# Kernel optimization log

Hardware: AMD Instinct MI355X
Metric: run time of the kernel (lower is better)

Reference implementation:

```python
import jax, jax.numpy as jnp
import numpy as np

N = 12288
D = 128
NUM_BATCH = 32
EPS = 1e-8


def setup_inputs() -> dict:
    key = jax.random.key(0)
    kq, kk, kv, kb = jax.random.split(key, 4)
    Q = jax.random.normal(kq, (N, D), dtype=jnp.float32)
    K = jax.random.normal(kk, (N, D), dtype=jnp.float32)
    V = jax.random.normal(kv, (N, D), dtype=jnp.float32)
    batch_seg = jnp.sort(jax.random.randint(kb, (N,), 0, NUM_BATCH, dtype=jnp.int32))
    return {"Q": Q, "K": K, "V": V, "num_batch": NUM_BATCH, "batch_seg": batch_seg}


def reference(Q, K, V, num_batch, batch_seg):
    d = Q.shape[-1]
    dot = Q @ K.T                                   # [N, N]
    # NOTE: faithful to original: subtract GLOBAL max, then divide by sqrt(d)
    A = jnp.exp((dot - jnp.max(dot)) / jnp.sqrt(jnp.float32(d)))
    if num_batch > 1:
        mask = (batch_seg[None, :] == batch_seg[:, None])  # block-diagonal
        A = jnp.where(mask, A, jnp.zeros((), A.dtype))
    norm = jnp.sum(A, axis=-1, keepdims=True) + EPS
    A_weights = A / norm
    return A_weights @ V
```

## Files before the change

kernel.cpp:

```cpp
#include <hip/hip_runtime.h>


#define NN 12288
#define DD 128
#define NB 32
#define PS_LD 40
#define VTS 12424

typedef __attribute__((ext_vector_type(8))) short short8;
typedef __attribute__((ext_vector_type(4))) float float4v;

__device__ __forceinline__ short f2bf(float f) {
  unsigned u = __builtin_bit_cast(unsigned, f);
  return (short)((u + 0x7FFFu + ((u >> 16) & 1u)) >> 16);
}

__device__ __forceinline__ short8 ld8_bf16(const float* p) {
  float4v f0 = *(const float4v*)p;
  float4v f1 = *(const float4v*)(p + 4);
  short8 s;
  s[0] = f2bf(f0[0]); s[1] = f2bf(f0[1]); s[2] = f2bf(f0[2]); s[3] = f2bf(f0[3]);
  s[4] = f2bf(f1[0]); s[5] = f2bf(f1[1]); s[6] = f2bf(f1[2]); s[7] = f2bf(f1[3]);
  return s;
}

__global__ __launch_bounds__(256) void prep_kernel(
    const float* __restrict__ K, const float* __restrict__ V,
    const int* __restrict__ seg,
    short* __restrict__ Kb, short* __restrict__ Vtb, int* __restrict__ starts) {
  const int tid = threadIdx.x;
  const int b = blockIdx.x;
  if (b < 768) {
    const size_t base = (size_t)b * 2048 + (size_t)tid * 8;
    *(short8*)(Kb + base) = ld8_bf16(K + base);
  } else if (b < 864) {
    __shared__ __align__(16) short Ts[DD * 136];
    const int kt = (b - 768) * 128;
#pragma unroll
    for (int rep = 0; rep < 16; ++rep) {
      int v = rep * 256 + tid;
      int key = v >> 5, c4 = (v & 31) * 4;
      float4v f = *(const float4v*)(V + (size_t)(kt + key) * DD + c4);
      Ts[(c4 + 0) * 136 + key] = f2bf(f[0]);
      Ts[(c4 + 1) * 136 + key] = f2bf(f[1]);
      Ts[(c4 + 2) * 136 + key] = f2bf(f[2]);
      Ts[(c4 + 3) * 136 + key] = f2bf(f[3]);
    }
    __syncthreads();
    const int c16 = (tid & 15) * 8;
#pragma unroll
    for (int rep = 0; rep < 8; ++rep) {
      int d = rep * 16 + (tid >> 4);
      short8 s = *(const short8*)&Ts[d * 136 + c16];
      *(short8*)(Vtb + (size_t)d * VTS + kt + c16) = s;
    }
  } else {
    int i = (b - 864) * 256 + tid;
    int s = seg[i];
    int sp = (i == 0) ? -1 : seg[i - 1];
    for (int bb = sp + 1; bb <= s; ++bb) starts[bb] = i;
    if (i == NN - 1)
      for (int bb = s + 1; bb <= NB; ++bb) starts[bb] = NN;
  }
}

struct Frags {
  short8 k0[4];
  short8 k1[4];
  short8 v[8];
};

__device__ __forceinline__ void load_frags(
    const short* __restrict__ Kb, const short* __restrict__ Vtb,
    int j0, int c, int quad, Frags& f) {
  const short* ka = Kb + (size_t)(j0 + c) * DD + quad * 8;
  const short* kb = ka + 16 * DD;
#pragma unroll
  for (int kc = 0; kc < 4; ++kc) {
    f.k0[kc] = *(const short8*)(ka + kc * 32);
    f.k1[kc] = *(const short8*)(kb + kc * 32);
  }
  const short* vb = Vtb + (size_t)c * VTS + j0 + quad * 8;
#pragma unroll
  for (int n = 0; n < 8; ++n)
    f.v[n] = *(const short8*)(vb + (size_t)n * 16 * VTS);
}

__global__ __launch_bounds__(256, 2) void attn_kernel(
    const float* __restrict__ Q, const short* __restrict__ Kb,
    const short* __restrict__ Vtb, const int* __restrict__ seg,
    const int* __restrict__ starts, float* __restrict__ out) {
  __shared__ __align__(16) short Ps[4][16 * PS_LD];
  __shared__ __align__(16) float Osc[4][16 * DD];
  __shared__ float Ls[4][16];

  const int tid = threadIdx.x;
  const int wave = tid >> 6;
  const int lane = tid & 63;
  const int c = lane & 15;
  const int quad = lane >> 4;

  const int bid = blockIdx.x;
  const int rg = (bid & 7) * 96 + (bid >> 3);
  const int i0 = rg * 16;

  const int segLoRow = seg[i0], segHiRow = seg[i0 + 15];
  const int lo = starts[segLoRow] & ~31;
  const int hi = starts[segHiRow + 1];

  int st_r[4], en_r[4];
#pragma unroll
  for (int r = 0; r < 4; ++r) {
    int s = seg[i0 + quad * 4 + r];
    st_r[r] = starts[s];
    en_r[r] = starts[s + 1];
  }

  short8 qf[4];
  {
    const float* qrow = Q + (size_t)(i0 + c) * DD + quad * 8;
#pragma unroll
    for (int kc = 0; kc < 4; ++kc) qf[kc] = ld8_bf16(qrow + kc * 32);
  }

  float4v acc[8];
#pragma unroll
  for (int n = 0; n < 8; ++n) acc[n] = (float4v){0.f, 0.f, 0.f, 0.f};
  float l_part[4] = {0.f, 0.f, 0.f, 0.f};

  const float scale = 0.08838834764831845f;

  int j0 = lo + wave * 32;
  if (j0 < hi) {
    Frags cur, nxt;
    load_frags(Kb, Vtb, j0, c, quad, cur);
    while (j0 < hi) {
      const int jn = j0 + 128;
      const int jl = (jn < hi) ? jn : j0;
      load_frags(Kb, Vtb, jl, c, quad, nxt);

      float4v s0 = (float4v){0.f, 0.f, 0.f, 0.f};
      float4v s1 = (float4v){0.f, 0.f, 0.f, 0.f};
#pragma unroll
      for (int kc = 0; kc < 4; ++kc) {
        s0 = __builtin_amdgcn_mfma_f32_16x16x32_bf16(qf[kc], cur.k0[kc], s0, 0, 0, 0);
        s1 = __builtin_amdgcn_mfma_f32_16x16x32_bf16(qf[kc], cur.k1[kc], s1, 0, 0, 0);
      }
      const int ja = j0 + c, jb = ja + 16;
      short* prow = &Ps[wave][0];
#pragma unroll
      for (int r = 0; r < 4; ++r) {
        float pa = (ja >= st_r[r] && ja < en_r[r]) ? __expf(s0[r] * scale) : 0.f;
        float pb = (jb >= st_r[r] && jb < en_r[r]) ? __expf(s1[r] * scale) : 0.f;
        l_part[r] += pa + pb;
        int row = quad * 4 + r;
        prow[row * PS_LD + c]      = f2bf(pa);
        prow[row * PS_LD + 16 + c] = f2bf(pb);
      }
      short8 pf = *(const short8*)&Ps[wave][c * PS_LD + quad * 8];
#pragma unroll
      for (int n = 0; n < 8; ++n)
        acc[n] = __builtin_amdgcn_mfma_f32_16x16x32_bf16(pf, cur.v[n], acc[n], 0, 0, 0);

      cur = nxt;
      j0 = jn;
    }
  }

  float lrow[4];
#pragma unroll
  for (int r = 0; r < 4; ++r) {
    float l = l_part[r];
    l += __shfl_xor(l, 1, 64);
    l += __shfl_xor(l, 2, 64);
    l += __shfl_xor(l, 4, 64);
    l += __shfl_xor(l, 8, 64);
    lrow[r] = l;
  }

#pragma unroll
  for (int n = 0; n < 8; ++n)
#pragma unroll
    for (int r = 0; r < 4; ++r)
      Osc[wave][(quad * 4 + r) * DD + n * 16 + c] = acc[n][r];
  if (c == 0) {
#pragma unroll
    for (int r = 0; r < 4; ++r) Ls[wave][quad * 4 + r] = lrow[r];
  }
  __syncthreads();

#pragma unroll
  for (int rep = 0; rep < 2; ++rep) {
    int e4 = rep * 256 + tid;
    int row = e4 >> 5, c4 = (e4 & 31) * 4;
    float l = Ls[0][row] + Ls[1][row] + Ls[2][row] + Ls[3][row];
    float4v o = (float4v){0.f, 0.f, 0.f, 0.f};
#pragma unroll
    for (int w = 0; w < 4; ++w) {
      float4v t = *(const float4v*)&Osc[w][row * DD + c4];
      o[0] += t[0]; o[1] += t[1]; o[2] += t[2]; o[3] += t[3];
    }
    float inv = 1.f / (l + 1e-8f);
    o[0] *= inv; o[1] *= inv; o[2] *= inv; o[3] *= inv;
    *(float4v*)(out + (size_t)(i0 + row) * DD + c4) = o;
  }
}

#define KT_LD 136
#define VT_LD 40
typedef __attribute__((ext_vector_type(4))) short short4v;

__global__ __launch_bounds__(256) void attn_fallback(
    const float* __restrict__ Q, const float* __restrict__ K,
    const float* __restrict__ V, const int* __restrict__ seg,
    float* __restrict__ out) {
  __shared__ __align__(16) short Kt[32 * KT_LD];
  __shared__ __align__(16) short Vt[DD * VT_LD];
  __shared__ __align__(16) short Ps[4][16 * PS_LD];
  const int tid = threadIdx.x, wave = tid >> 6, lane = tid & 63;
  const int c = lane & 15, quad = lane >> 4;
  const int m0 = blockIdx.x * 64, i0 = m0 + wave * 16;
  const int segFirst = seg[m0], segLast = seg[m0 + 63];
  int lo = 0, hb = NN;
  while (lo < hb) { int mid = (lo + hb) >> 1; if (seg[mid] < segFirst) lo = mid + 1; else hb = mid; }
  int hi = lo, hb2 = NN;
  while (hi < hb2) { int mid = (hi + hb2) >> 1; if (seg[mid] <= segLast) hi = mid + 1; else hb2 = mid; }
  short8 qf[4];
  const float* qrow = Q + (size_t)(i0 + c) * DD + quad * 8;
#pragma unroll
  for (int kc = 0; kc < 4; ++kc) qf[kc] = ld8_bf16(qrow + kc * 32);
  int seg_r[4];
#pragma unroll
  for (int r = 0; r < 4; ++r) seg_r[r] = seg[i0 + quad * 4 + r];
  float4v acc[8];
#pragma unroll
  for (int n = 0; n < 8; ++n) acc[n] = (float4v){0.f, 0.f, 0.f, 0.f};
  float l_part[4] = {0.f, 0.f, 0.f, 0.f};
  const float scale = 0.08838834764831845f;
  for (int j0 = lo; j0 < hi; j0 += 32) {
    __syncthreads();
    {
      int row = tid >> 3, ch = tid & 7;
      int jj = j0 + row; if (jj > NN - 1) jj = NN - 1;
      const float* kp = K + (size_t)jj * DD + ch * 16;
      short* dst = &Kt[row * KT_LD + ch * 16];
#pragma unroll
      for (int q4 = 0; q4 < 4; ++q4) {
        float4v f = *(const float4v*)(kp + q4 * 4);
        short4v s;
        s[0] = f2bf(f[0]); s[1] = f2bf(f[1]); s[2] = f2bf(f[2]); s[3] = f2bf(f[3]);
        *(short4v*)(dst + q4 * 4) = s;
      }
    }
    {
      int d = tid & 127, jh = tid >> 7;
      float vv[16];
#pragma unroll
      for (int j = 0; j < 16; ++j) {
        int jj = j0 + jh * 16 + j; if (jj > NN - 1) jj = NN - 1;
        vv[j] = V[(size_t)jj * DD + d];
      }
      short8 a, b2;
#pragma unroll
      for (int j = 0; j < 8; ++j) { a[j] = f2bf(vv[j]); b2[j] = f2bf(vv[8 + j]); }
      *(short8*)&Vt[d * VT_LD + jh * 16] = a;
      *(short8*)&Vt[d * VT_LD + jh * 16 + 8] = b2;
    }
    __syncthreads();
    float4v s0 = (float4v){0.f, 0.f, 0.f, 0.f};
    float4v s1 = (float4v){0.f, 0.f, 0.f, 0.f};
    const short* krow0 = &Kt[c * KT_LD + quad * 8];
    const short* krow1 = &Kt[(16 + c) * KT_LD + quad * 8];
#pragma unroll
    for (int kc = 0; kc < 4; ++kc) {
      short8 b0 = *(const short8*)(krow0 + kc * 32);
      short8 b1 = *(const short8*)(krow1 + kc * 32);
      s0 = __builtin_amdgcn_mfma_f32_16x16x32_bf16(qf[kc], b0, s0, 0, 0, 0);
      s1 = __builtin_amdgcn_mfma_f32_16x16x32_bf16(qf[kc], b1, s1, 0, 0, 0);
    }
    int ja = j0 + c, jb = ja + 16;
    int sa = seg[ja < NN ? ja : NN - 1];
    int sb = seg[jb < NN ? jb : NN - 1];
    bool va = ja < hi, vb = jb < hi;
    short* prow = &Ps[wave][0];
#pragma unroll
    for (int r = 0; r < 4; ++r) {
      float pa = (va && sa == seg_r[r]) ? __expf(s0[r] * scale) : 0.f;
      float pb = (vb && sb == seg_r[r]) ? __expf(s1[r] * scale) : 0.f;
      l_part[r] += pa + pb;
      int row = quad * 4 + r;
      prow[row * PS_LD + c] = f2bf(pa);
      prow[row * PS_LD + 16 + c] = f2bf(pb);
    }
    short8 pf = *(const short8*)&Ps[wave][c * PS_LD + quad * 8];
#pragma unroll
    for (int n = 0; n < 8; ++n) {
      short8 vfr = *(const short8*)&Vt[(n * 16 + c) * VT_LD + quad * 8];
      acc[n] = __builtin_amdgcn_mfma_f32_16x16x32_bf16(pf, vfr, acc[n], 0, 0, 0);
    }
  }
  float linv[4];
#pragma unroll
  for (int r = 0; r < 4; ++r) {
    float l = l_part[r];
    l += __shfl_xor(l, 1, 64);
    l += __shfl_xor(l, 2, 64);
    l += __shfl_xor(l, 4, 64);
    l += __shfl_xor(l, 8, 64);
    linv[r] = 1.f / (l + 1e-8f);
  }
#pragma unroll
  for (int n = 0; n < 8; ++n)
#pragma unroll
    for (int r = 0; r < 4; ++r)
      out[(size_t)(i0 + quad * 4 + r) * DD + n * 16 + c] = acc[n][r] * linv[r];
}

extern "C" void kernel_launch(void* const* d_in, const int* in_sizes, int n_in,
                              void* d_out, int out_size, void* d_ws, size_t ws_size,
                              hipStream_t stream) {
  const float* Q = (const float*)d_in[0];
  const float* K = (const float*)d_in[1];
  const float* V = (const float*)d_in[2];
  const int* seg = (const int*)d_in[4];
  float* out = (float*)d_out;

  const size_t kb_bytes = (size_t)NN * DD * sizeof(short);
  const size_t vt_bytes = (size_t)DD * VTS * sizeof(short);
  const size_t need = kb_bytes + vt_bytes + 64 * sizeof(int);

  if (ws_size >= need) {
    short* Kb = (short*)d_ws;
    short* Vtb = (short*)((char*)d_ws + kb_bytes);
    int* starts = (int*)((char*)d_ws + kb_bytes + vt_bytes);
    prep_kernel<<<864 + NN / 256, 256, 0, stream>>>(K, V, seg, Kb, Vtb, starts);
    attn_kernel<<<NN / 16, 256, 0, stream>>>(Q, Kb, Vtb, seg, starts, out);
  } else {
    attn_fallback<<<NN / 64, 256, 0, stream>>>(Q, K, V, seg, out);
  }
}
```

Baseline: 106.8 us.

## Share K/V tiles across 64-row blocks via LDS DMA and split keys

Each block now covers 64 query rows (16 per wave) and stages 32-key K and V^T tiles into swizzled LDS with global_load_lds double buffering, so all four waves reuse each tile instead of each wave loading its own fragments from global memory. The key range is split four ways across blocks, and partial outputs and row sums go to a workspace that a new combine kernel reduces and normalises. This cuts redundant global K/V traffic and improves load balance. In exchange it adds an extra kernel launch, a block-wide barrier per tile, and a large fp32 partial-output write and read.

Result: faster. 96.40 us (-9.7%).

```diff
diff --git a/kernel.cpp b/kernel.cpp
--- a/kernel.cpp
+++ b/kernel.cpp
@@ -22,6 +22,12 @@
   s[0] = f2bf(f0[0]); s[1] = f2bf(f0[1]); s[2] = f2bf(f0[2]); s[3] = f2bf(f0[3]);
   s[4] = f2bf(f1[0]); s[5] = f2bf(f1[1]); s[6] = f2bf(f1[2]); s[7] = f2bf(f1[3]);
   return s;
+}
+
+__device__ __forceinline__ void dma16(const short* gsrc, short* ldst) {
+  auto g = (const __attribute__((address_space(1))) void*)(unsigned long long)gsrc;
+  auto l = (__attribute__((address_space(3))) void*)(unsigned)(unsigned long long)ldst;
+  __builtin_amdgcn_global_load_lds(g, l, 16, 0, 0);
 }
 
 __global__ __launch_bounds__(256) void prep_kernel(
@@ -64,35 +70,33 @@
   }
 }
 
-struct Frags {
-  short8 k0[4];
-  short8 k1[4];
-  short8 v[8];
-};
-
-__device__ __forceinline__ void load_frags(
+__device__ __forceinline__ void issue_tile(
     const short* __restrict__ Kb, const short* __restrict__ Vtb,
-    int j0, int c, int quad, Frags& f) {
-  const short* ka = Kb + (size_t)(j0 + c) * DD + quad * 8;
-  const short* kb = ka + 16 * DD;
-#pragma unroll
-  for (int kc = 0; kc < 4; ++kc) {
-    f.k0[kc] = *(const short8*)(ka + kc * 32);
-    f.k1[kc] = *(const short8*)(kb + kc * 32);
-  }
-  const short* vb = Vtb + (size_t)c * VTS + j0 + quad * 8;
-#pragma unroll
-  for (int n = 0; n < 8; ++n)
-    f.v[n] = *(const short8*)(vb + (size_t)n * 16 * VTS);
-}
-
-__global__ __launch_bounds__(256, 2) void attn_kernel(
+    short* KshP, short* VshP, int j0, int wave, int lane) {
+#pragma unroll
+  for (int i = 0; i < 2; ++i) {
+    const int R = wave * 8 + i * 4;
+    const int row = R + (lane >> 4);
+    const int dchunk = (lane & 15) ^ (row & 15);
+    dma16(Kb + (size_t)(j0 + row) * DD + dchunk * 8, KshP + R * 128);
+  }
+#pragma unroll
+  for (int i = 0; i < 2; ++i) {
+    const int D = wave * 32 + i * 16;
+    const int dr = D + (lane >> 2);
+    const int vchunk = (lane & 3) ^ ((lane >> 2) & 3);
+    dma16(Vtb + (size_t)dr * VTS + j0 + vchunk * 8, VshP + D * 32);
+  }
+}
+
+__global__ __launch_bounds__(256, 3) void attn_kernel(
     const float* __restrict__ Q, const short* __restrict__ Kb,
     const short* __restrict__ Vtb, const int* __restrict__ seg,
-    const int* __restrict__ starts, float* __restrict__ out) {
+    const int* __restrict__ starts,
+    float* __restrict__ Op, float* __restrict__ lp) {
+  __shared__ __align__(16) short Ksh[2][32 * 128];
+  __shared__ __align__(16) short Vsh[2][128 * 32];
   __shared__ __align__(16) short Ps[4][16 * PS_LD];
-  __shared__ __align__(16) float Osc[4][16 * DD];
-  __shared__ float Ls[4][16];
 
   const int tid = threadIdx.x;
   const int wave = tid >> 6;
@@ -101,24 +105,31 @@
   const int quad = lane >> 4;
 
   const int bid = blockIdx.x;
-  const int rg = (bid & 7) * 96 + (bid >> 3);
-  const int i0 = rg * 16;
-
-  const int segLoRow = seg[i0], segHiRow = seg[i0 + 15];
-  const int lo = starts[segLoRow] & ~31;
-  const int hi = starts[segHiRow + 1];
+  const int y = bid >> 3;
+  const int rg = (bid & 7) * 24 + (y >> 2);
+  const int sk = y & 3;
+  const int i0 = rg * 64;
+  const int i0w = i0 + wave * 16;
+
+  const int L = starts[seg[i0]];
+  const int H = starts[seg[i0 + 63] + 1];
+  const int Lm = L & ~31;
+  const int nck = (H - Lm + 31) >> 5;
+  const int ck0 = (nck * sk) >> 2;
+  const int ck1 = (nck * (sk + 1)) >> 2;
+  const int nt = ck1 - ck0;
 
   int st_r[4], en_r[4];
 #pragma unroll
   for (int r = 0; r < 4; ++r) {
-    int s = seg[i0 + quad * 4 + r];
+    int s = seg[i0w + quad * 4 + r];
     st_r[r] = starts[s];
     en_r[r] = starts[s + 1];
   }
 
   short8 qf[4];
   {
-    const float* qrow = Q + (size_t)(i0 + c) * DD + quad * 8;
+    const float* qrow = Q + (size_t)(i0w + c) * DD + quad * 8;
 #pragma unroll
     for (int kc = 0; kc < 4; ++kc) qf[kc] = ld8_bf16(qrow + kc * 32);
   }
@@ -130,41 +141,50 @@
 
   const float scale = 0.08838834764831845f;
 
-  int j0 = lo + wave * 32;
-  if (j0 < hi) {
-    Frags cur, nxt;
-    load_frags(Kb, Vtb, j0, c, quad, cur);
-    while (j0 < hi) {
-      const int jn = j0 + 128;
-      const int jl = (jn < hi) ? jn : j0;
-      load_frags(Kb, Vtb, jl, c, quad, nxt);
-
-      float4v s0 = (float4v){0.f, 0.f, 0.f, 0.f};
-      float4v s1 = (float4v){0.f, 0.f, 0.f, 0.f};
-#pragma unroll
-      for (int kc = 0; kc < 4; ++kc) {
-        s0 = __builtin_amdgcn_mfma_f32_16x16x32_bf16(qf[kc], cur.k0[kc], s0, 0, 0, 0);
-        s1 = __builtin_amdgcn_mfma_f32_16x16x32_bf16(qf[kc], cur.k1[kc], s1, 0, 0, 0);
-      }
-      const int ja = j0 + c, jb = ja + 16;
-      short* prow = &Ps[wave][0];
-#pragma unroll
-      for (int r = 0; r < 4; ++r) {
-        float pa = (ja >= st_r[r] && ja < en_r[r]) ? __expf(s0[r] * scale) : 0.f;
-        float pb = (jb >= st_r[r] && jb < en_r[r]) ? __expf(s1[r] * scale) : 0.f;
-        l_part[r] += pa + pb;
-        int row = quad * 4 + r;
-        prow[row * PS_LD + c]      = f2bf(pa);
-        prow[row * PS_LD + 16 + c] = f2bf(pb);
-      }
-      short8 pf = *(const short8*)&Ps[wave][c * PS_LD + quad * 8];
-#pragma unroll
-      for (int n = 0; n < 8; ++n)
-        acc[n] = __builtin_amdgcn_mfma_f32_16x16x32_bf16(pf, cur.v[n], acc[n], 0, 0, 0);
-
-      cur = nxt;
-      j0 = jn;
-    }
+  if (nt > 0)
+    issue_tile(Kb, Vtb, &Ksh[0][0], &Vsh[0][0], Lm + ck0 * 32, wave, lane);
+  __syncthreads();
+
+  for (int t = 0; t < nt; ++t) {
+    const int j0 = Lm + (ck0 + t) * 32;
+    const int p = t & 1;
+    if (t + 1 < nt)
+      issue_tile(Kb, Vtb, &Ksh[p ^ 1][0], &Vsh[p ^ 1][0], j0 + 32, wave, lane);
+
+    float4v s0 = (float4v){0.f, 0.f, 0.f, 0.f};
+    float4v s1 = (float4v){0.f, 0.f, 0.f, 0.f};
+    const short* Kp = &Ksh[p][0];
+#pragma unroll
+    for (int kc = 0; kc < 4; ++kc) {
+      const int pos = ((kc * 4 + quad) ^ c) * 8;
+      short8 b0 = *(const short8*)(Kp + c * 128 + pos);
+      short8 b1 = *(const short8*)(Kp + (16 + c) * 128 + pos);
+      s0 = __builtin_amdgcn_mfma_f32_16x16x32_bf16(qf[kc], b0, s0, 0, 0, 0);
+      s1 = __builtin_amdgcn_mfma_f32_16x16x32_bf16(qf[kc], b1, s1, 0, 0, 0);
+    }
+
+    const int ja = j0 + c, jb = ja + 16;
+    short* prow = &Ps[wave][0];
+#pragma unroll
+    for (int r = 0; r < 4; ++r) {
+      float pa = (ja >= st_r[r] && ja < en_r[r]) ? __expf(s0[r] * scale) : 0.f;
+      float pb = (jb >= st_r[r] && jb < en_r[r]) ? __expf(s1[r] * scale) : 0.f;
+      l_part[r] += pa + pb;
+      int row = quad * 4 + r;
+      prow[row * PS_LD + c]      = f2bf(pa);
+      prow[row * PS_LD + 16 + c] = f2bf(pb);
+    }
+    short8 pf = *(const short8*)&Ps[wave][c * PS_LD + quad * 8];
+
+    const short* Vp = &Vsh[p][0];
+    const int vpos = (quad ^ (c & 3)) * 8;
+#pragma unroll
+    for (int n = 0; n < 8; ++n) {
+      short8 vf = *(const short8*)(Vp + (n * 16 + c) * 32 + vpos);
+      acc[n] = __builtin_amdgcn_mfma_f32_16x16x32_bf16(pf, vf, acc[n], 0, 0, 0);
+    }
+
+    __syncthreads();
   }
 
   float lrow[4];
@@ -178,31 +198,36 @@
     lrow[r] = l;
   }
 
+  float* OpW = Op + ((size_t)sk * NN + i0w) * DD;
 #pragma unroll
   for (int n = 0; n < 8; ++n)
 #pragma unroll
     for (int r = 0; r < 4; ++r)
-      Osc[wave][(quad * 4 + r) * DD + n * 16 + c] = acc[n][r];
+      OpW[(quad * 4 + r) * DD + n * 16 + c] = acc[n][r];
   if (c == 0) {
 #pragma unroll
-    for (int r = 0; r < 4; ++r) Ls[wave][quad * 4 + r] = lrow[r];
-  }
-  __syncthreads();
-
+    for (int r = 0; r < 4; ++r) lp[sk * NN + i0w + quad * 4 + r] = lrow[r];
+  }
+}
+
+__global__ __launch_bounds__(256) void combine_kernel(
+    const float* __restrict__ Op, const float* __restrict__ lp,
+    float* __restrict__ out) {
+  const int idx = blockIdx.x * 256 + threadIdx.x;
 #pragma unroll
   for (int rep = 0; rep < 2; ++rep) {
-    int e4 = rep * 256 + tid;
-    int row = e4 >> 5, c4 = (e4 & 31) * 4;
-    float l = Ls[0][row] + Ls[1][row] + Ls[2][row] + Ls[3][row];
+    int u = idx + rep * 196608;
+    int row = u >> 5, c4 = (u & 31) * 4;
+    float l = lp[row] + lp[NN + row] + lp[2 * NN + row] + lp[3 * NN + row];
     float4v o = (float4v){0.f, 0.f, 0.f, 0.f};
 #pragma unroll
-    for (int w = 0; w < 4; ++w) {
-      float4v t = *(const float4v*)&Osc[w][row * DD + c4];
+    for (int s = 0; s < 4; ++s) {
+      float4v t = *(const float4v*)(Op + ((size_t)s * NN + row) * DD + c4);
       o[0] += t[0]; o[1] += t[1]; o[2] += t[2]; o[3] += t[3];
     }
     float inv = 1.f / (l + 1e-8f);
     o[0] *= inv; o[1] *= inv; o[2] *= inv; o[3] *= inv;
-    *(float4v*)(out + (size_t)(i0 + row) * DD + c4) = o;
+    *(float4v*)(out + (size_t)row * DD + c4) = o;
   }
 }
 
@@ -327,14 +352,21 @@
 
   const size_t kb_bytes = (size_t)NN * DD * sizeof(short);
   const size_t vt_bytes = (size_t)DD * VTS * sizeof(short);
-  const size_t need = kb_bytes + vt_bytes + 64 * sizeof(int);
+  const size_t st_bytes = 64 * sizeof(int);
+  const size_t op_bytes = (size_t)4 * NN * DD * sizeof(float);
+  const size_t lp_bytes = (size_t)4 * NN * sizeof(float);
+  const size_t need = kb_bytes + vt_bytes + st_bytes + op_bytes + lp_bytes;
 
   if (ws_size >= need) {
-    short* Kb = (short*)d_ws;
-    short* Vtb = (short*)((char*)d_ws + kb_bytes);
-    int* starts = (int*)((char*)d_ws + kb_bytes + vt_bytes);
+    char* w = (char*)d_ws;
+    short* Kb  = (short*)w;                     w += kb_bytes;
+    short* Vtb = (short*)w;                     w += vt_bytes;
+    int* starts = (int*)w;                      w += st_bytes;
+    float* Op = (float*)w;                      w += op_bytes;
+    float* lp = (float*)w;
     prep_kernel<<<864 + NN / 256, 256, 0, stream>>>(K, V, seg, Kb, Vtb, starts);
-    attn_kernel<<<NN / 16, 256, 0, stream>>>(Q, Kb, Vtb, seg, starts, out);
+    attn_kernel<<<768, 256, 0, stream>>>(Q, Kb, Vtb, seg, starts, Op, lp);
+    combine_kernel<<<768, 256, 0, stream>>>(Op, lp, out);
   } else {
     attn_fallback<<<NN / 64, 256, 0, stream>>>(Q, K, V, seg, out);
   }
```
